# Kernel tuning notes

Measured on AMD Instinct MI355X. Metric: run time of the kernel, lower is better.

The kernel has to match this reference:

```python
import jax, jax.numpy as jnp
import numpy as np

D = 192          # d_model
H = 8            # n_heads
DH = D // H      # d_head = 24
DFF = 2 * D      # FeedForward hidden = d_model*2
SIZES = [384 + 8 * i for i in range(32)]   # ragged segment lengths
TOTAL = sum(SIZES)                          # 16256
EPS = 1e-5

# static ragged -> padded index maps (numpy, baked at trace time)
_sz = np.asarray(SIZES)
B = len(_sz)
MAXN = int(_sz.max())
SEG = np.repeat(np.arange(B), _sz)                      # [TOTAL] segment id
POS = np.concatenate([np.arange(s) for s in _sz])       # [TOTAL] position in segment
PADMASK = np.ones((B, MAXN), dtype=bool)                # True = padding (key_padding_mask)
PADMASK[SEG, POS] = False


def _layernorm(x, gamma, beta):
    mu = jnp.mean(x, axis=-1, keepdims=True)
    var = jnp.var(x, axis=-1, keepdims=True)
    return (x - mu) * jax.lax.rsqrt(var + EPS) * gamma + beta


def setup_inputs() -> dict:
    key = jax.random.key(0)
    ks = jax.random.split(key, 8)
    w = lambda k, shape: jax.random.normal(k, shape, jnp.float32) * 0.02
    return {
        "x": jax.random.normal(ks[0], (TOTAL, D), jnp.float32),
        "sizes": jnp.asarray(SIZES, jnp.int32),
        "Wqkv": w(ks[1], (3 * D, D)), "bqkv": jnp.zeros((3 * D,), jnp.float32),
        "Wo": w(ks[2], (D, D)),       "bo": jnp.zeros((D,), jnp.float32),
        "Wg": w(ks[3], (D, 2 * D)),   "bg": jnp.zeros((D,), jnp.float32),
        "gamma1": jnp.ones((D,), jnp.float32), "beta1": jnp.zeros((D,), jnp.float32),
        "W1": w(ks[4], (DFF, D)),     "b1": jnp.zeros((DFF,), jnp.float32),
        "W2": w(ks[5], (D, DFF)),     "b2": jnp.zeros((D,), jnp.float32),
        "gamma2": jnp.ones((D,), jnp.float32), "beta2": jnp.zeros((D,), jnp.float32),
    }


def reference(x, sizes, Wqkv, bqkv, Wo, bo, Wg, bg, gamma1, beta1,
              W1, b1, W2, b2, gamma2, beta2):
    # --- pad_by_sizes (vectorized scatter, static index maps) ---
    pad = jnp.zeros((B, MAXN, D), x.dtype).at[SEG, POS].set(x)   # [B, MAXN, D]

    # --- nn.MultiheadAttention (batch_first, key_padding_mask) ---
    qkv = pad @ Wqkv.T + bqkv                                    # [B, MAXN, 3D]
    q, k, v = jnp.split(qkv, 3, axis=-1)
    def heads(t):  # [B, MAXN, D] -> [B, H, MAXN, DH]
        return t.reshape(B, MAXN, H, DH).transpose(0, 2, 1, 3)
    q, k, v = heads(q), heads(k), heads(v)
    scores = jnp.einsum("bhqd,bhkd->bhqk", q, k) / np.sqrt(DH)   # [B, H, MAXN, MAXN]
    scores = jnp.where(PADMASK[:, None, None, :], jnp.float32(-1e9), scores)
    attn = jax.nn.softmax(scores, axis=-1)
    o = jnp.einsum("bhqk,bhkd->bhqd", attn, v)                   # [B, H, MAXN, DH]
    o = o.transpose(0, 2, 1, 3).reshape(B, MAXN, D)
    out = o @ Wo.T + bo                                          # [B, MAXN, D]

    # --- gather back to ragged; gate/norm/ff are per-token, so the torch
    # per-segment loop is equivalent to one vectorized pass over all tokens ---
    out_flat = out[SEG, POS]                                     # [TOTAL, D]
    g = jax.nn.sigmoid(jnp.concatenate([out_flat, x], axis=-1) @ Wg.T + bg)
    h = g * out_flat + (1.0 - g) * x                             # GatedResidual
    h = _layernorm(h, gamma1, beta1)                             # self.norm
    y = jax.nn.silu(h @ W1.T + b1) @ W2.T + b2                   # FeedForward.net
    return _layernorm(h + y, gamma2, beta2)                      # residual + norm
```

## Files before the change

kernel.cpp:

```cpp
#include <hip/hip_runtime.h>
#include <math.h>

#define D_      192
#define H_      8
#define DH_     24
#define NSEG    32
#define TOTAL_  16256
static constexpr float LN_EPS = 1e-5f;
static constexpr float SCALE  = 0.20412414523193154f;
static constexpr float SC_L2E = 0.29446679331797463f;

typedef float  f32x4  __attribute__((ext_vector_type(4)));
typedef short  bf16x8 __attribute__((ext_vector_type(8)));
typedef unsigned short u16x4 __attribute__((ext_vector_type(4)));
typedef unsigned int   u32x4 __attribute__((ext_vector_type(4)));

__device__ __forceinline__ unsigned short f2b(float f) {
    union { float f; unsigned u; } v; v.f = f;
    unsigned r = v.u + 0x7FFFu + ((v.u >> 16) & 1u);
    return (unsigned short)(r >> 16);
}
__device__ __forceinline__ unsigned f2b_u32(float f) {
    union { float f; unsigned u; } v; v.f = f;
    return (v.u + 0x8000u) >> 16;
}
__device__ __forceinline__ unsigned short f2b_fast(float f) {
    union { float f; unsigned u; } v; v.f = f;
    return (unsigned short)((v.u + 0x8000u) >> 16);
}
__device__ __forceinline__ float b2f(unsigned short h) {
    union { unsigned u; float f; } v; v.u = (unsigned)h << 16; return v.f;
}
__device__ __forceinline__ float fexp2(float x) {
#if __has_builtin(__builtin_amdgcn_exp2f)
    return __builtin_amdgcn_exp2f(x);
#else
    return exp2f(x);
#endif
}

#define NXE 3121152
__global__ __launch_bounds__(256)
void conv_all(const float* __restrict__ x,
              const float* __restrict__ w0, const float* __restrict__ w1,
              const float* __restrict__ w2, const float* __restrict__ w3,
              const float* __restrict__ w4,
              unsigned short* __restrict__ xb, unsigned short* __restrict__ wb)
{
    int i = (blockIdx.x * 256 + threadIdx.x) * 4;
    const float* src; unsigned short* dst; int off;
    if (i < NXE) { src = x; dst = xb; off = 0; }
    else {
        int j = i - NXE; dst = wb;
        if      (j < 110592) { src = w0; off = 0; }
        else if (j < 147456) { src = w1; off = 110592; }
        else if (j < 221184) { src = w2; off = 147456; }
        else if (j < 294912) { src = w3; off = 221184; }
        else                 { src = w4; off = 294912; }
        i = j;
    }
    float4 v = *(const float4*)&src[i - off];
    u16x4 o = { f2b(v.x), f2b(v.y), f2b(v.z), f2b(v.w) };
    *(u16x4*)&dst[i] = o;
}

template<int KF, int MR, int OUT_BF16>
__global__ __launch_bounds__(256)
void gemm_lds(const unsigned short* __restrict__ Ain,
              const unsigned short* __restrict__ Wb,
              const float* __restrict__ bias,
              void* __restrict__ Cout, int N)
{
    constexpr int KSW = KF * 32 + 8;
    __shared__ unsigned short Wp[64 * KSW];

    const int tid = threadIdx.x;
    const int wv  = tid >> 6;
    const int l   = tid & 63;
    const int m0  = blockIdx.x * (64 * MR) + wv * (16 * MR);
    const int n0  = blockIdx.y * 64;
    const int rl  = l & 15;
    const int kc  = (l >> 4) * 8;

    bf16x8 afrag[MR][KF];
    #pragma unroll
    for (int h = 0; h < MR; ++h)
        #pragma unroll
        for (int kk = 0; kk < KF; ++kk)
            afrag[h][kk] = *(const bf16x8*)&Ain[(size_t)(m0 + h * 16 + rl) * (KF * 32) + kk * 32 + kc];

    #pragma unroll
    for (int i = 0; i < KF; ++i) {
        int u = i * 256 + tid;
        int row = u / (KF * 4), c = u % (KF * 4);
        *(bf16x8*)&Wp[row * KSW + c * 8] = *(const bf16x8*)&Wb[(size_t)(n0 + row) * (KF * 32) + c * 8];
    }
    __syncthreads();

    f32x4 acc[MR][4] = {};
    #pragma unroll
    for (int kk = 0; kk < KF; ++kk) {
        #pragma unroll
        for (int nf = 0; nf < 4; ++nf) {
            bf16x8 b = *(const bf16x8*)&Wp[(nf * 16 + rl) * KSW + kk * 32 + kc];
            #pragma unroll
            for (int h = 0; h < MR; ++h)
                acc[h][nf] = __builtin_amdgcn_mfma_f32_16x16x32_bf16(afrag[h][kk], b, acc[h][nf], 0, 0, 0);
        }
    }

    #pragma unroll
    for (int h = 0; h < MR; ++h) {
        #pragma unroll
        for (int nf = 0; nf < 4; ++nf) {
            const int c = n0 + nf * 16 + rl;
            const float bz = bias[c];
            #pragma unroll
            for (int q = 0; q < 4; ++q) {
                const int r = m0 + h * 16 + (l >> 4) * 4 + q;
                float v = acc[h][nf][q] + bz;
                if (OUT_BF16) ((unsigned short*)Cout)[(size_t)r * N + c] = f2b(v);
                else          ((float*)Cout)[(size_t)r * N + c] = v;
            }
        }
    }
}

__global__ __launch_bounds__(256, 2)
void tail_fused(const unsigned short* __restrict__ o_b,
                const unsigned short* __restrict__ xb,
                const unsigned short* __restrict__ wo_b,
                const unsigned short* __restrict__ wg_b,
                const unsigned short* __restrict__ w1_b,
                const unsigned short* __restrict__ w2_b,
                const float* __restrict__ bo, const float* __restrict__ bg,
                const float* __restrict__ b1, const float* __restrict__ b2,
                const float* __restrict__ gamma1, const float* __restrict__ beta1,
                const float* __restrict__ gamma2, const float* __restrict__ beta2,
                float* __restrict__ out)
{
    constexpr int WS = 200;
    __shared__ unsigned short Wp[96 * WS];
    __shared__ unsigned short Al[64 * WS];

    const int tid = threadIdx.x;
    const int wv  = tid >> 6;
    const int l   = tid & 63;
    const int rl  = l & 15;
    const int g   = l >> 4;
    const int kc  = g * 8;
    const int m0  = blockIdx.x * 64 + wv * 16;

    bf16x8 afA[6];
    #pragma unroll
    for (int kk = 0; kk < 6; ++kk)
        afA[kk] = *(const bf16x8*)&o_b[(size_t)(m0 + rl) * 192 + kk * 32 + kc];

    f32x4 accA[12] = {};
    #pragma unroll
    for (int sub = 0; sub < 2; ++sub) {
        __syncthreads();
        #pragma unroll
        for (int i = 0; i < 9; ++i) {
            int u = i * 256 + tid;
            int row = u / 24, c = u % 24;
            *(bf16x8*)&Wp[row * WS + c * 8] = *(const bf16x8*)&wo_b[(size_t)(sub * 96 + row) * 192 + c * 8];
        }
        __syncthreads();
        #pragma unroll
        for (int kk = 0; kk < 6; ++kk)
            #pragma unroll
            for (int nf2 = 0; nf2 < 6; ++nf2) {
                bf16x8 b = *(const bf16x8*)&Wp[(nf2 * 16 + rl) * WS + kk * 32 + kc];
                accA[sub * 6 + nf2] = __builtin_amdgcn_mfma_f32_16x16x32_bf16(afA[kk], b, accA[sub * 6 + nf2], 0, 0, 0);
            }
    }

    float att[12][4];
    #pragma unroll
    for (int nf = 0; nf < 12; ++nf) {
        const int cnf = (nf / 6) * 96 + (nf % 6) * 16 + rl;
        const float bz = bo[cnf];
        #pragma unroll
        for (int q = 0; q < 4; ++q) {
            att[nf][q] = accA[nf][q] + bz;
            Al[(wv * 16 + g * 4 + q) * WS + cnf] = f2b(att[nf][q]);
        }
    }

    bf16x8 afX[6];
    #pragma unroll
    for (int kk = 0; kk < 6; ++kk)
        afX[kk] = *(const bf16x8*)&xb[(size_t)(m0 + rl) * 192 + kk * 32 + kc];

    f32x4 accB[12] = {};
    #pragma unroll
    for (int kb = 0; kb < 2; ++kb)
        #pragma unroll
        for (int sub = 0; sub < 2; ++sub) {
            __syncthreads();
            #pragma unroll
            for (int i = 0; i < 9; ++i) {
                int u = i * 256 + tid;
                int row = u / 24, c = u % 24;
                *(bf16x8*)&Wp[row * WS + c * 8] = *(const bf16x8*)&wg_b[(size_t)(sub * 96 + row) * 384 + kb * 192 + c * 8];
            }
            __syncthreads();
            #pragma unroll
            for (int kk = 0; kk < 6; ++kk) {
                bf16x8 a = (kb == 0) ? *(const bf16x8*)&Al[(wv * 16 + rl) * WS + kk * 32 + kc]
                                     : afX[kk];
                #pragma unroll
                for (int nf2 = 0; nf2 < 6; ++nf2) {
                    bf16x8 b = *(const bf16x8*)&Wp[(nf2 * 16 + rl) * WS + kk * 32 + kc];
                    accB[sub * 6 + nf2] = __builtin_amdgcn_mfma_f32_16x16x32_bf16(a, b, accB[sub * 6 + nf2], 0, 0, 0);
                }
            }
        }

    float h1ln[12][4];
    {
        float bz[12], gam[12], bet[12];
        #pragma unroll
        for (int nf = 0; nf < 12; ++nf) {
            const int cnf = (nf / 6) * 96 + (nf % 6) * 16 + rl;
            bz[nf]  = bg[cnf];
            gam[nf] = gamma1[cnf];
            bet[nf] = beta1[cnf];
        }
        #pragma unroll
        for (int q = 0; q < 4; ++q) {
            const int r = m0 + g * 4 + q;
            const size_t rb = (size_t)r * 192;
            float h[12];
            float s = 0.f;
            #pragma unroll
            for (int nf = 0; nf < 12; ++nf) {
                const int cnf = (nf / 6) * 96 + (nf % 6) * 16 + rl;
                float v  = accB[nf][q] + bz[nf];
                float gt = 1.f / (1.f + __expf(-v));
                h[nf] = gt * att[nf][q] + (1.f - gt) * b2f(xb[rb + cnf]);
                s += h[nf];
            }
            s += __shfl_xor(s, 1); s += __shfl_xor(s, 2);
            s += __shfl_xor(s, 4); s += __shfl_xor(s, 8);
            const float mu = s * (1.f / 192.f);
            float sq = 0.f;
            #pragma unroll
            for (int nf = 0; nf < 12; ++nf) { float d = h[nf] - mu; sq += d * d; }
            sq += __shfl_xor(sq, 1); sq += __shfl_xor(sq, 2);
            sq += __shfl_xor(sq, 4); sq += __shfl_xor(sq, 8);
            const float rstd = rsqrtf(sq * (1.f / 192.f) + LN_EPS);
            #pragma unroll
            for (int nf = 0; nf < 12; ++nf)
                h1ln[nf][q] = (h[nf] - mu) * rstd * gam[nf] + bet[nf];
        }
    }
    __syncthreads();
    #pragma unroll
    for (int nf = 0; nf < 12; ++nf) {
        const int cnf = (nf / 6) * 96 + (nf % 6) * 16 + rl;
        #pragma unroll
        for (int q = 0; q < 4; ++q)
            Al[(wv * 16 + g * 4 + q) * WS + cnf] = f2b(h1ln[nf][q]);
    }
    __syncthreads();

    bf16x8 afC[6];
    #pragma unroll
    for (int kk = 0; kk < 6; ++kk)
        afC[kk] = *(const bf16x8*)&Al[(wv * 16 + rl) * WS + kk * 32 + kc];

    f32x4 accD[12] = {};
    #pragma unroll
    for (int ch = 0; ch < 2; ++ch) {
        f32x4 accC[12] = {};
        #pragma unroll
        for (int sub = 0; sub < 2; ++sub) {
            __syncthreads();
            #pragma unroll
            for (int i = 0; i < 9; ++i) {
                int u = i * 256 + tid;
                int row = u / 24, c = u % 24;
                *(bf16x8*)&Wp[row * WS + c * 8] = *(const bf16x8*)&w1_b[(size_t)(ch * 192 + sub * 96 + row) * 192 + c * 8];
            }
            __syncthreads();
            #pragma unroll
            for (int kk = 0; kk < 6; ++kk)
                #pragma unroll
                for (int nf2 = 0; nf2 < 6; ++nf2) {
                    bf16x8 b = *(const bf16x8*)&Wp[(nf2 * 16 + rl) * WS + kk * 32 + kc];
                    accC[sub * 6 + nf2] = __builtin_amdgcn_mfma_f32_16x16x32_bf16(afC[kk], b, accC[sub * 6 + nf2], 0, 0, 0);
                }
        }
        __syncthreads();
        #pragma unroll
        for (int nf = 0; nf < 12; ++nf) {
            const int colc = (nf / 6) * 96 + (nf % 6) * 16 + rl;
            const float bz1 = b1[ch * 192 + colc];
            #pragma unroll
            for (int q = 0; q < 4; ++q) {
                float v = accC[nf][q] + bz1;
                float s = 1.f / (1.f + __expf(-v));
                Al[(wv * 16 + g * 4 + q) * WS + colc] = f2b(v * s);
            }
        }
        #pragma unroll
        for (int sub = 0; sub < 2; ++sub) {
            __syncthreads();
            #pragma unroll
            for (int i = 0; i < 9; ++i) {
                int u = i * 256 + tid;
                int row = u / 24, c = u % 24;
                *(bf16x8*)&Wp[row * WS + c * 8] = *(const bf16x8*)&w2_b[(size_t)(sub * 96 + row) * 384 + ch * 192 + c * 8];
            }
            __syncthreads();
            #pragma unroll
            for (int kk = 0; kk < 6; ++kk) {
                bf16x8 a = *(const bf16x8*)&Al[(wv * 16 + rl) * WS + kk * 32 + kc];
                #pragma unroll
                for (int nf2 = 0; nf2 < 6; ++nf2) {
                    bf16x8 b = *(const bf16x8*)&Wp[(nf2 * 16 + rl) * WS + kk * 32 + kc];
                    accD[sub * 6 + nf2] = __builtin_amdgcn_mfma_f32_16x16x32_bf16(a, b, accD[sub * 6 + nf2], 0, 0, 0);
                }
            }
        }
    }

    float bz[12], gam[12], bet[12];
    #pragma unroll
    for (int nf = 0; nf < 12; ++nf) {
        const int cnf = (nf / 6) * 96 + (nf % 6) * 16 + rl;
        bz[nf]  = b2[cnf];
        gam[nf] = gamma2[cnf];
        bet[nf] = beta2[cnf];
    }
    #pragma unroll
    for (int q = 0; q < 4; ++q) {
        const int r = m0 + g * 4 + q;
        const size_t rb = (size_t)r * 192;
        float h[12];
        float s = 0.f;
        #pragma unroll
        for (int nf = 0; nf < 12; ++nf) {
            h[nf] = h1ln[nf][q] + accD[nf][q] + bz[nf];
            s += h[nf];
        }
        s += __shfl_xor(s, 1); s += __shfl_xor(s, 2);
        s += __shfl_xor(s, 4); s += __shfl_xor(s, 8);
        const float mu = s * (1.f / 192.f);
        float sq = 0.f;
        #pragma unroll
        for (int nf = 0; nf < 12; ++nf) { float d = h[nf] - mu; sq += d * d; }
        sq += __shfl_xor(sq, 1); sq += __shfl_xor(sq, 2);
        sq += __shfl_xor(sq, 4); sq += __shfl_xor(sq, 8);
        const float rstd = rsqrtf(sq * (1.f / 192.f) + LN_EPS);
        #pragma unroll
        for (int nf = 0; nf < 12; ++nf) {
            const int cnf = (nf / 6) * 96 + (nf % 6) * 16 + rl;
            out[rb + cnf] = (h[nf] - mu) * rstd * gam[nf] + bet[nf];
        }
    }
}

#define KSTR 40
#define VSTR 72

__global__ __launch_bounds__(256)
void attn_mfma(const unsigned short* __restrict__ qkv, unsigned short* __restrict__ o)
{
    const int w    = blockIdx.x;
    const int xcd  = w & 7;
    const int slot = w >> 3;
    const int seg  = xcd + 8 * (slot / 80);
    const int inr  = slot % 80;
    const int head = inr / 10;
    const int q0   = (inr % 10) * 64;

    const int n    = 384 + 8 * seg;
    const int base = 384 * seg + 4 * seg * (seg - 1);
    if (q0 >= n) return;

    __shared__ unsigned short Ks[2][64 * KSTR];
    __shared__ unsigned short Vt[2][32 * VSTR];

    const int tid = threadIdx.x;
    const int wv  = tid >> 6;
    const int l   = tid & 63;
    const int lq  = l & 15;
    const int g   = l >> 4;

    if (tid < 64) {
        *(uint4*)&Ks[0][tid * KSTR + 24] = make_uint4(0, 0, 0, 0);
        *(uint4*)&Ks[1][tid * KSTR + 24] = make_uint4(0, 0, 0, 0);
    }
    for (int t4 = tid; t4 < 144; t4 += 256) {
        *(unsigned long long*)&Vt[0][24 * VSTR + t4 * 4] = 0ull;
        *(unsigned long long*)&Vt[1][24 * VSTR + t4 * 4] = 0ull;
    }

    const int qrow = q0 + wv * 16 + lq;
    const int qtok = base + (qrow < n ? qrow : n - 1);
    bf16x8 qfrag = {};
    if (g < 3) qfrag = *(const bf16x8*)&qkv[(size_t)qtok * 576 + head * 24 + g * 8];

    const int sj  = tid & 63;
    const int sc  = tid >> 6;
    const int scj = 32 * (sj >> 5) + 8 * ((sj >> 2) & 3) + 4 * ((sj >> 4) & 1) + (sj & 3);

    bf16x8 kreg = {}, vreg = {};
    if (tid < 192) {
        int jr = sj; if (jr >= n) jr = n - 1;
        const unsigned short* rp = &qkv[(size_t)(base + jr) * 576 + head * 24 + sc * 8];
        kreg = *(const bf16x8*)(rp + 192);
        vreg = *(const bf16x8*)(rp + 384);
        *(bf16x8*)&Ks[0][sj * KSTR + sc * 8] = kreg;
        #pragma unroll
        for (int e = 0; e < 8; ++e)
            Vt[0][(sc * 8 + e) * VSTR + scj] = ((const unsigned short*)&vreg)[e];
    }

    float lsum = 0.f;
    f32x4 oacc[2] = {};

    const int nt = (n + 63) >> 6;
    int cur = 0;
    for (int t = 0; t < nt; ++t) {
        __syncthreads();
        const int j0 = t * 64;
        const bool pf = (t + 1 < nt) && (tid < 192);
        if (pf) {
            int jr = j0 + 64 + sj; if (jr >= n) jr = n - 1;
            const unsigned short* rp = &qkv[(size_t)(base + jr) * 576 + head * 24 + sc * 8];
            kreg = *(const bf16x8*)(rp + 192);
            vreg = *(const bf16x8*)(rp + 384);
        }

        bf16x8 kf[4];
        #pragma unroll
        for (int ks = 0; ks < 4; ++ks)
            kf[ks] = *(const bf16x8*)&Ks[cur][(ks * 16 + lq) * KSTR + g * 8];

        const int rem = n - j0;
        f32x4 sacc[4] = {};
        #pragma unroll
        for (int ks = 0; ks < 4; ++ks)
            sacc[ks] = __builtin_amdgcn_mfma_f32_16x16x32_bf16(kf[ks], qfrag, sacc[ks], 0, 0, 0);

        float psum = 0.f;
        unsigned pw[8];
        #pragma unroll
        for (int ks = 0; ks < 4; ++ks) {
            float pv[4];
            #pragma unroll
            for (int r = 0; r < 4; ++r) {
                float p = fexp2(sacc[ks][r] * SC_L2E);
                if (rem < 64) { int key = ks * 16 + g * 4 + r; if (key >= rem) p = 0.f; }
                psum += p;
                pv[r] = p;
            }
            pw[ks * 2 + 0] = f2b_u32(pv[0]) | (f2b_u32(pv[1]) << 16);
            pw[ks * 2 + 1] = f2b_u32(pv[2]) | (f2b_u32(pv[3]) << 16);
        }
        psum += __shfl_xor(psum, 16);
        psum += __shfl_xor(psum, 32);
        lsum += psum;

        bf16x8 pfr[2];
        #pragma unroll
        for (int jk = 0; jk < 2; ++jk) {
            u32x4 fr = { pw[jk*4+0], pw[jk*4+1], pw[jk*4+2], pw[jk*4+3] };
            pfr[jk] = *(bf16x8*)&fr;
        }

        #pragma unroll
        for (int jk = 0; jk < 2; ++jk) {
            #pragma unroll
            for (int df = 0; df < 2; ++df) {
                bf16x8 vf = *(const bf16x8*)&Vt[cur][(df * 16 + lq) * VSTR + jk * 32 + g * 8];
                oacc[df] = __builtin_amdgcn_mfma_f32_16x16x32_bf16(vf, pfr[jk], oacc[df], 0, 0, 0);
            }
        }

        if (pf) {
            *(bf16x8*)&Ks[cur ^ 1][sj * KSTR + sc * 8] = kreg;
            #pragma unroll
            for (int e = 0; e < 8; ++e)
                Vt[cur ^ 1][(sc * 8 + e) * VSTR + scj] = ((const unsigned short*)&vreg)[e];
        }
        cur ^= 1;
    }

    if (qrow < n) {
        const float rl2 = 1.f / lsum;
        #pragma unroll
        for (int df = 0; df < 2; ++df) {
            const int d0 = df * 16 + g * 4;
            if (d0 < 24) {
                u16x4 r = { f2b_fast(oacc[df][0] * rl2), f2b_fast(oacc[df][1] * rl2),
                            f2b_fast(oacc[df][2] * rl2), f2b_fast(oacc[df][3] * rl2) };
                *(u16x4*)&o[(size_t)(base + qrow) * 192 + head * 24 + d0] = r;
            }
        }
    }
}

extern "C" void kernel_launch(void* const* d_in, const int* in_sizes, int n_in,
                              void* d_out, int out_size, void* d_ws, size_t ws_size,
                              hipStream_t stream)
{
    const float* x      = (const float*)d_in[0];
    const float* Wqkv   = (const float*)d_in[2];
    const float* bqkv   = (const float*)d_in[3];
    const float* Wo     = (const float*)d_in[4];
    const float* bo     = (const float*)d_in[5];
    const float* Wg     = (const float*)d_in[6];
    const float* bg     = (const float*)d_in[7];
    const float* gamma1 = (const float*)d_in[8];
    const float* beta1  = (const float*)d_in[9];
    const float* W1     = (const float*)d_in[10];
    const float* b1     = (const float*)d_in[11];
    const float* W2     = (const float*)d_in[12];
    const float* b2     = (const float*)d_in[13];
    const float* gamma2 = (const float*)d_in[14];
    const float* beta2  = (const float*)d_in[15];
    float* out = (float*)d_out;
    float* ws  = (float*)d_ws;

    const size_t T = TOTAL_;
    unsigned short* qkv_b = (unsigned short*)ws;
    unsigned short* o_b   = (unsigned short*)(ws + 288 * T);
    unsigned short* wb    = (unsigned short*)(ws + 384 * T);
    unsigned short* xb    = (unsigned short*)(ws + 396 * T);

    dim3 blk(256);

    conv_all<<<dim3(3408), blk, 0, stream>>>(x, Wqkv, Wo, Wg, W1, W2, xb, wb);
    gemm_lds<6,2,1><<<dim3(127, 9), blk, 0, stream>>>(xb, wb, bqkv, qkv_b, 576);
    attn_mfma<<<dim3(2560), blk, 0, stream>>>(qkv_b, o_b);
    tail_fused<<<dim3(254), blk, 0, stream>>>(o_b, xb, wb + 110592, wb + 147456,
                                              wb + 221184, wb + 294912,
                                              bo, bg, b1, b2,
                                              gamma1, beta1, gamma2, beta2, out);
}
```

Before: 90.65 us.

## Fuse x fp32-to-bf16 conversion into QKV GEMM and loop over output bands

Result: slower. 94.47 us (+4.2%).

```diff
diff --git a/kernel.cpp b/kernel.cpp
--- a/kernel.cpp
+++ b/kernel.cpp
@@ -38,89 +38,86 @@
     return exp2f(x);
 #endif
 }
-
-#define NXE 3121152
+__device__ __forceinline__ bf16x8 ldpack8(const float* p) {
+    float4 a0 = *(const float4*)p;
+    float4 a1 = *(const float4*)(p + 4);
+    bf16x8 r;
+    ((unsigned short*)&r)[0] = f2b(a0.x); ((unsigned short*)&r)[1] = f2b(a0.y);
+    ((unsigned short*)&r)[2] = f2b(a0.z); ((unsigned short*)&r)[3] = f2b(a0.w);
+    ((unsigned short*)&r)[4] = f2b(a1.x); ((unsigned short*)&r)[5] = f2b(a1.y);
+    ((unsigned short*)&r)[6] = f2b(a1.z); ((unsigned short*)&r)[7] = f2b(a1.w);
+    return r;
+}
+
 __global__ __launch_bounds__(256)
-void conv_all(const float* __restrict__ x,
-              const float* __restrict__ w0, const float* __restrict__ w1,
-              const float* __restrict__ w2, const float* __restrict__ w3,
-              const float* __restrict__ w4,
-              unsigned short* __restrict__ xb, unsigned short* __restrict__ wb)
+void conv_w(const float* __restrict__ w0, const float* __restrict__ w1,
+            const float* __restrict__ w2, const float* __restrict__ w3,
+            const float* __restrict__ w4, unsigned short* __restrict__ out)
 {
     int i = (blockIdx.x * 256 + threadIdx.x) * 4;
-    const float* src; unsigned short* dst; int off;
-    if (i < NXE) { src = x; dst = xb; off = 0; }
-    else {
-        int j = i - NXE; dst = wb;
-        if      (j < 110592) { src = w0; off = 0; }
-        else if (j < 147456) { src = w1; off = 110592; }
-        else if (j < 221184) { src = w2; off = 147456; }
-        else if (j < 294912) { src = w3; off = 221184; }
-        else                 { src = w4; off = 294912; }
-        i = j;
-    }
+    const float* src; int off;
+    if      (i < 110592) { src = w0; off = 0; }
+    else if (i < 147456) { src = w1; off = 110592; }
+    else if (i < 221184) { src = w2; off = 147456; }
+    else if (i < 294912) { src = w3; off = 221184; }
+    else                 { src = w4; off = 294912; }
     float4 v = *(const float4*)&src[i - off];
     u16x4 o = { f2b(v.x), f2b(v.y), f2b(v.z), f2b(v.w) };
-    *(u16x4*)&dst[i] = o;
-}
-
-template<int KF, int MR, int OUT_BF16>
+    *(u16x4*)&out[i] = o;
+}
+
 __global__ __launch_bounds__(256)
-void gemm_lds(const unsigned short* __restrict__ Ain,
-              const unsigned short* __restrict__ Wb,
-              const float* __restrict__ bias,
-              void* __restrict__ Cout, int N)
+void gemm_qkv_fused(const float* __restrict__ x,
+                    const unsigned short* __restrict__ Wb,
+                    const float* __restrict__ bias,
+                    unsigned short* __restrict__ qkv_b,
+                    unsigned short* __restrict__ xb)
 {
-    constexpr int KSW = KF * 32 + 8;
+    constexpr int KSW = 200;
     __shared__ unsigned short Wp[64 * KSW];
 
     const int tid = threadIdx.x;
     const int wv  = tid >> 6;
     const int l   = tid & 63;
-    const int m0  = blockIdx.x * (64 * MR) + wv * (16 * MR);
-    const int n0  = blockIdx.y * 64;
     const int rl  = l & 15;
-    const int kc  = (l >> 4) * 8;
-
-    bf16x8 afrag[MR][KF];
-    #pragma unroll
-    for (int h = 0; h < MR; ++h)
-        #pragma unroll
-        for (int kk = 0; kk < KF; ++kk)
-            afrag[h][kk] = *(const bf16x8*)&Ain[(size_t)(m0 + h * 16 + rl) * (KF * 32) + kk * 32 + kc];
-
-    #pragma unroll
-    for (int i = 0; i < KF; ++i) {
-        int u = i * 256 + tid;
-        int row = u / (KF * 4), c = u % (KF * 4);
-        *(bf16x8*)&Wp[row * KSW + c * 8] = *(const bf16x8*)&Wb[(size_t)(n0 + row) * (KF * 32) + c * 8];
-    }
-    __syncthreads();
-
-    f32x4 acc[MR][4] = {};
-    #pragma unroll
-    for (int kk = 0; kk < KF; ++kk) {
+    const int g   = l >> 4;
+    const int kc  = g * 8;
+    const int m0  = blockIdx.x * 64 + wv * 16;
+
+    bf16x8 afrag[6];
+    #pragma unroll
+    for (int kk = 0; kk < 6; ++kk) {
+        afrag[kk] = ldpack8(&x[(size_t)(m0 + rl) * 192 + kk * 32 + kc]);
+        *(bf16x8*)&xb[(size_t)(m0 + rl) * 192 + kk * 32 + kc] = afrag[kk];
+    }
+
+    for (int band = 0; band < 9; ++band) {
+        __syncthreads();
+        #pragma unroll
+        for (int i = 0; i < 6; ++i) {
+            int u = i * 256 + tid;
+            int row = u / 24, c = u % 24;
+            *(bf16x8*)&Wp[row * KSW + c * 8] = *(const bf16x8*)&Wb[(size_t)(band * 64 + row) * 192 + c * 8];
+        }
+        __syncthreads();
+
+        f32x4 acc[4] = {};
+        #pragma unroll
+        for (int kk = 0; kk < 6; ++kk)
+            #pragma unroll
+            for (int nf = 0; nf < 4; ++nf) {
+                bf16x8 b = *(const bf16x8*)&Wp[(nf * 16 + rl) * KSW + kk * 32 + kc];
+                acc[nf] = __builtin_amdgcn_mfma_f32_16x16x32_bf16(afrag[kk], b, acc[nf], 0, 0, 0);
+            }
+
         #pragma unroll
         for (int nf = 0; nf < 4; ++nf) {
-            bf16x8 b = *(const bf16x8*)&Wp[(nf * 16 + rl) * KSW + kk * 32 + kc];
-            #pragma unroll
-            for (int h = 0; h < MR; ++h)
-                acc[h][nf] = __builtin_amdgcn_mfma_f32_16x16x32_bf16(afrag[h][kk], b, acc[h][nf], 0, 0, 0);
-        }
-    }
-
-    #pragma unroll
-    for (int h = 0; h < MR; ++h) {
-        #pragma unroll
-        for (int nf = 0; nf < 4; ++nf) {
-            const int c = n0 + nf * 16 + rl;
+            const int c = band * 64 + nf * 16 + rl;
             const float bz = bias[c];
             #pragma unroll
             for (int q = 0; q < 4; ++q) {
-                const int r = m0 + h * 16 + (l >> 4) * 4 + q;
-                float v = acc[h][nf][q] + bz;
-                if (OUT_BF16) ((unsigned short*)Cout)[(size_t)r * N + c] = f2b(v);
-                else          ((float*)Cout)[(size_t)r * N + c] = v;
+                const int r = m0 + g * 4 + q;
+                qkv_b[(size_t)r * 576 + c] = f2b(acc[nf][q] + bz);
             }
         }
     }
@@ -195,7 +192,7 @@
 
     f32x4 accB[12] = {};
     #pragma unroll
-    for (int kb = 0; kb < 2; ++kb)
+    for (int kb2 = 0; kb2 < 2; ++kb2)
         #pragma unroll
         for (int sub = 0; sub < 2; ++sub) {
             __syncthreads();
@@ -203,13 +200,13 @@
             for (int i = 0; i < 9; ++i) {
                 int u = i * 256 + tid;
                 int row = u / 24, c = u % 24;
-                *(bf16x8*)&Wp[row * WS + c * 8] = *(const bf16x8*)&wg_b[(size_t)(sub * 96 + row) * 384 + kb * 192 + c * 8];
+                *(bf16x8*)&Wp[row * WS + c * 8] = *(const bf16x8*)&wg_b[(size_t)(sub * 96 + row) * 384 + kb2 * 192 + c * 8];
             }
             __syncthreads();
             #pragma unroll
             for (int kk = 0; kk < 6; ++kk) {
-                bf16x8 a = (kb == 0) ? *(const bf16x8*)&Al[(wv * 16 + rl) * WS + kk * 32 + kc]
-                                     : afX[kk];
+                bf16x8 a = (kb2 == 0) ? *(const bf16x8*)&Al[(wv * 16 + rl) * WS + kk * 32 + kc]
+                                      : afX[kk];
                 #pragma unroll
                 for (int nf2 = 0; nf2 < 6; ++nf2) {
                     bf16x8 b = *(const bf16x8*)&Wp[(nf2 * 16 + rl) * WS + kk * 32 + kc];
@@ -535,8 +532,8 @@
 
     dim3 blk(256);
 
-    conv_all<<<dim3(3408), blk, 0, stream>>>(x, Wqkv, Wo, Wg, W1, W2, xb, wb);
-    gemm_lds<6,2,1><<<dim3(127, 9), blk, 0, stream>>>(xb, wb, bqkv, qkv_b, 576);
+    conv_w<<<dim3(360), blk, 0, stream>>>(Wqkv, Wo, Wg, W1, W2, wb);
+    gemm_qkv_fused<<<dim3(254), blk, 0, stream>>>(x, wb, bqkv, qkv_b, xb);
     attn_mfma<<<dim3(2560), blk, 0, stream>>>(qkv_b, o_b);
     tail_fused<<<dim3(254), blk, 0, stream>>>(o_b, xb, wb + 110592, wb + 147456,
                                               wb + 221184, wb + 294912,
```
